# Optimization experiments

Hardware: AMD Instinct MI355X
Metric: run time of the kernel (lower is better)

Reference implementation:

```python
import jax, jax.numpy as jnp
import numpy as np

MARGIN = 1.0
GAMMA = 0.9
B, L, DATA_LEN = 512, 100, 100000


def setup_inputs() -> dict:
    key = jax.random.key(0)
    k1, k2, k3, k4 = jax.random.split(key, 4)
    y_pred = jax.random.normal(k1, (B, L), dtype=jnp.float32)
    # multilabel targets in {0,1}; guarantee >=1 positive per label (torch asserts this)
    y_true = (jax.random.uniform(k2, (B, L)) < 0.3).astype(jnp.float32)
    y_true = y_true.at[0, :].set(1.0)
    # unique dataset sample ids for this minibatch
    index = jnp.arange(B, dtype=jnp.int32)
    # EMA buffers (num_labels, data_len, 1); positive values emulate a warm state
    u_all = jax.random.uniform(k3, (L, DATA_LEN, 1), jnp.float32, 0.1, 1.0)
    u_pos = jax.random.uniform(k4, (L, DATA_LEN, 1), jnp.float32, 0.05, 0.5)
    return {"y_pred": y_pred, "y_true": y_true, "index": index,
            "u_all": u_all, "u_pos": u_pos}


def reference(y_pred, y_true, index, u_all, u_pos):
    # pos[l, b] = 1 if sample b is positive for label l
    pos = (y_true == 1.0).astype(y_pred.dtype).T          # (L, B)
    fp = y_pred.T                                          # (L, B)
    # pairwise surrogate: squared hinge of margin - (f_ps - f_all), all rows;
    # rows for negative samples are masked out below (torch only keeps pos rows)
    diff = fp[:, :, None] - fp[:, None, :]                 # (L, B, B)
    sur = jnp.square(jnp.maximum(MARGIN - diff, 0.0))      # (L, B, B)
    row_mean = jnp.mean(sur, axis=2)                       # (L, B)
    pos_row_mean = jnp.mean(sur * pos[:, None, :], axis=2) # (L, B)
    # gather EMA state for this minibatch, update only at positive rows (detached)
    ua = u_all[:, index, 0]                                # (L, B)
    up = u_pos[:, index, 0]                                # (L, B)
    ua_new = jnp.where(pos > 0, (1.0 - GAMMA) * ua + GAMMA * jax.lax.stop_gradient(row_mean), ua)
    up_new = jnp.where(pos > 0, (1.0 - GAMMA) * up + GAMMA * jax.lax.stop_gradient(pos_row_mean), up)
    # p_i = (u_pos - u_all * pos_mask) / u_all**2, shape (P, B) in torch -> masked (L, B, B)
    denom = jnp.where(pos > 0, ua_new, 1.0)                # guard masked rows
    p_i = (up_new[:, :, None] - ua_new[:, :, None] * pos[:, None, :]) / jnp.square(denom)[:, :, None]
    p_i = jax.lax.stop_gradient(p_i)
    n_pos = jnp.sum(pos, axis=1)                           # (L,) positives per label
    b = y_pred.shape[0]
    # torch: loss_l = mean over (P_l, B) of p_i * sur_loss; average over labels
    per_label = jnp.sum(p_i * sur * pos[:, :, None], axis=(1, 2)) / (n_pos * b)
    return jnp.mean(per_label)
```

## Files before the change

### kernel.cpp

```cpp
#include <hip/hip_runtime.h>

#define BB 512
#define LL 100
#define DLEN 100000

__global__ __launch_bounds__(BB) void map_loss_rows(
    const float* __restrict__ y_pred,
    const float* __restrict__ y_true,
    const int*   __restrict__ index,
    const float* __restrict__ u_all,
    const float* __restrict__ u_pos,
    double*      __restrict__ per_label
) {
    const int l = blockIdx.x;
    const int i = threadIdx.x;

    __shared__ float fp_s[BB];
    __shared__ float pos_s[BB];

    const float xi = y_pred[(size_t)i * LL + l];
    const float pi = (y_true[(size_t)i * LL + l] == 1.0f) ? 1.0f : 0.0f;
    fp_s[i]  = xi;
    pos_s[i] = pi;
    __syncthreads();

    float S = 0.0f, SP = 0.0f;
#pragma unroll 8
    for (int j = 0; j < BB; ++j) {
        const float d  = xi - fp_s[j];
        const float m  = 1.0f - d;
        const float mm = fmaxf(m, 0.0f);
        const float s  = mm * mm;
        S  += s;
        SP += s * pos_s[j];
    }

    double c = 0.0;
    if (pi > 0.0f) {
        const float row_mean     = S  * (1.0f / BB);
        const float pos_row_mean = SP * (1.0f / BB);
        const int   idx = index[i];
        const float ua  = u_all[(size_t)l * DLEN + idx];
        const float up  = u_pos[(size_t)l * DLEN + idx];
        const float ua_new = 0.1f * ua + 0.9f * row_mean;
        const float up_new = 0.1f * up + 0.9f * pos_row_mean;
        c = (double)((up_new * S - ua_new * SP) / (ua_new * ua_new));
    }

    double npos = (double)pi;
    for (int off = 32; off > 0; off >>= 1) {
        c    += __shfl_down(c, off, 64);
        npos += __shfl_down(npos, off, 64);
    }
    __shared__ double red_c[8];
    __shared__ double red_n[8];
    const int wave = i >> 6;
    const int lane = i & 63;
    if (lane == 0) { red_c[wave] = c; red_n[wave] = npos; }
    __syncthreads();
    if (i == 0) {
        double cs = 0.0, ns = 0.0;
#pragma unroll
        for (int w = 0; w < 8; ++w) { cs += red_c[w]; ns += red_n[w]; }
        per_label[l] = cs / (ns * (double)BB);
    }
}

__global__ __launch_bounds__(128) void map_loss_final(
    const double* __restrict__ per_label, float* __restrict__ out) {
    const int t = threadIdx.x;
    double v = (t < LL) ? per_label[t] : 0.0;
    for (int off = 32; off > 0; off >>= 1) v += __shfl_down(v, off, 64);
    __shared__ double tmp[2];
    if ((t & 63) == 0) tmp[t >> 6] = v;
    __syncthreads();
    if (t == 0) out[0] = (float)((tmp[0] + tmp[1]) / (double)LL);
}

extern "C" void kernel_launch(void* const* d_in, const int* in_sizes, int n_in,
                              void* d_out, int out_size, void* d_ws, size_t ws_size,
                              hipStream_t stream) {
    const float* y_pred = (const float*)d_in[0];
    const float* y_true = (const float*)d_in[1];
    const int*   index  = (const int*)d_in[2];
    const float* u_all  = (const float*)d_in[3];
    const float* u_pos  = (const float*)d_in[4];

    double* per_label = (double*)d_ws;
    float*  out       = (float*)d_out;

    map_loss_rows<<<LL, BB, 0, stream>>>(y_pred, y_true, index, u_all, u_pos, per_label);
    map_loss_final<<<1, 128, 0, stream>>>(per_label, out);
}
```

Measured before the change: 114.1 us.

## Fuse final reduction via atomicAdd and split each row across two threads

Merges the per-label and final reduction kernels into one kernel that accumulates each label's contribution into the output with a float atomicAdd, after a memset. Each row's inner loop over 512 columns is split between two threads of a 1024-thread block and recombined with a shuffle, doubling parallelism per block. The margin term is also folded into a single add. The cost is one extra memset launch and a float atomic whose result depends on the order the blocks finish.

```diff
diff --git a/kernel.cpp b/kernel.cpp
--- a/kernel.cpp
+++ b/kernel.cpp
@@ -4,77 +4,76 @@
 #define LL 100
 #define DLEN 100000
 
-__global__ __launch_bounds__(BB) void map_loss_rows(
+__global__ __launch_bounds__(1024) void map_loss_fused(
     const float* __restrict__ y_pred,
     const float* __restrict__ y_true,
     const int*   __restrict__ index,
     const float* __restrict__ u_all,
     const float* __restrict__ u_pos,
-    double*      __restrict__ per_label
-) {
+    float*       __restrict__ out)
+{
     const int l = blockIdx.x;
-    const int i = threadIdx.x;
+    const int t = threadIdx.x;
+    const int i = t >> 1;
+    const int h = t & 1;
 
     __shared__ float fp_s[BB];
     __shared__ float pos_s[BB];
 
-    const float xi = y_pred[(size_t)i * LL + l];
-    const float pi = (y_true[(size_t)i * LL + l] == 1.0f) ? 1.0f : 0.0f;
-    fp_s[i]  = xi;
-    pos_s[i] = pi;
+    if (t < BB) {
+        fp_s[t]  = y_pred[(size_t)t * LL + l];
+        pos_s[t] = (y_true[(size_t)t * LL + l] == 1.0f) ? 1.0f : 0.0f;
+    }
     __syncthreads();
 
+    const float xi = fp_s[i];
+    const float pi = pos_s[i];
+    const float tm = 1.0f - xi;
+
     float S = 0.0f, SP = 0.0f;
+    const int j0 = h * (BB / 2);
 #pragma unroll 8
-    for (int j = 0; j < BB; ++j) {
-        const float d  = xi - fp_s[j];
-        const float m  = 1.0f - d;
+    for (int j = j0; j < j0 + BB / 2; ++j) {
+        const float m  = tm + fp_s[j];
         const float mm = fmaxf(m, 0.0f);
         const float s  = mm * mm;
         S  += s;
         SP += s * pos_s[j];
     }
+    S  += __shfl_xor(S, 1, 64);
+    SP += __shfl_xor(SP, 1, 64);
 
-    double c = 0.0;
-    if (pi > 0.0f) {
-        const float row_mean     = S  * (1.0f / BB);
-        const float pos_row_mean = SP * (1.0f / BB);
-        const int   idx = index[i];
-        const float ua  = u_all[(size_t)l * DLEN + idx];
-        const float up  = u_pos[(size_t)l * DLEN + idx];
-        const float ua_new = 0.1f * ua + 0.9f * row_mean;
-        const float up_new = 0.1f * up + 0.9f * pos_row_mean;
-        c = (double)((up_new * S - ua_new * SP) / (ua_new * ua_new));
+    double c = 0.0, npos = 0.0;
+    if (h == 0) {
+        npos = (double)pi;
+        if (pi > 0.0f) {
+            const float row_mean     = S  * (1.0f / BB);
+            const float pos_row_mean = SP * (1.0f / BB);
+            const int   idx = index[i];
+            const float ua  = u_all[(size_t)l * DLEN + idx];
+            const float up  = u_pos[(size_t)l * DLEN + idx];
+            const float ua_new = 0.1f * ua + 0.9f * row_mean;
+            const float up_new = 0.1f * up + 0.9f * pos_row_mean;
+            c = (double)((up_new * S - ua_new * SP) / (ua_new * ua_new));
+        }
     }
 
-    double npos = (double)pi;
     for (int off = 32; off > 0; off >>= 1) {
         c    += __shfl_down(c, off, 64);
         npos += __shfl_down(npos, off, 64);
     }
-    __shared__ double red_c[8];
-    __shared__ double red_n[8];
-    const int wave = i >> 6;
-    const int lane = i & 63;
-    if (lane == 0) { red_c[wave] = c; red_n[wave] = npos; }
+    __shared__ double red_c[16];
+    __shared__ double red_n[16];
+    const int wave = t >> 6;
+    if ((t & 63) == 0) { red_c[wave] = c; red_n[wave] = npos; }
     __syncthreads();
-    if (i == 0) {
+    if (t == 0) {
         double cs = 0.0, ns = 0.0;
 #pragma unroll
-        for (int w = 0; w < 8; ++w) { cs += red_c[w]; ns += red_n[w]; }
-        per_label[l] = cs / (ns * (double)BB);
+        for (int w = 0; w < 16; ++w) { cs += red_c[w]; ns += red_n[w]; }
+        const float contrib = (float)(cs / (ns * (double)BB) / (double)LL);
+        atomicAdd(out, contrib);
     }
-}
-
-__global__ __launch_bounds__(128) void map_loss_final(
-    const double* __restrict__ per_label, float* __restrict__ out) {
-    const int t = threadIdx.x;
-    double v = (t < LL) ? per_label[t] : 0.0;
-    for (int off = 32; off > 0; off >>= 1) v += __shfl_down(v, off, 64);
-    __shared__ double tmp[2];
-    if ((t & 63) == 0) tmp[t >> 6] = v;
-    __syncthreads();
-    if (t == 0) out[0] = (float)((tmp[0] + tmp[1]) / (double)LL);
 }
 
 extern "C" void kernel_launch(void* const* d_in, const int* in_sizes, int n_in,
@@ -85,10 +84,8 @@
     const int*   index  = (const int*)d_in[2];
     const float* u_all  = (const float*)d_in[3];
     const float* u_pos  = (const float*)d_in[4];
+    float* out = (float*)d_out;
 
-    double* per_label = (double*)d_ws;
-    float*  out       = (float*)d_out;
-
-    map_loss_rows<<<LL, BB, 0, stream>>>(y_pred, y_true, index, u_all, u_pos, per_label);
-    map_loss_final<<<1, 128, 0, stream>>>(per_label, out);
+    hipMemsetAsync(out, 0, sizeof(float), stream);
+    map_loss_fused<<<LL, 1024, 0, stream>>>(y_pred, y_true, index, u_all, u_pos, out);
 }
```

Result: no change. 113.4 us (-0.6%).
